# Kernel tuning notes

Hardware: AMD Instinct MI355X
Metric: run time of the kernel (lower is better)

The kernel has to match this reference:

```python
import jax, jax.numpy as jnp
import numpy as np

N_NODES = 50000
N_EDGES = 800000
IN_DIM = 128
HID = 256
NUM_GRAPHS = 128


def setup_inputs() -> dict:
    key = jax.random.key(0)
    ks = jax.random.split(key, 12)
    x = jax.random.normal(ks[0], (N_NODES, IN_DIM), dtype=jnp.float32)
    edge_index = jax.random.randint(ks[1], (2, N_EDGES), 0, N_NODES, dtype=jnp.int32)
    batch = jnp.sort(jax.random.randint(ks[2], (N_NODES,), 0, NUM_GRAPHS, dtype=jnp.int32))
    def glorot(k, fan_in, fan_out):
        s = jnp.sqrt(6.0 / (fan_in + fan_out))
        return jax.random.uniform(k, (fan_in, fan_out), jnp.float32, -s, s)
    W1 = glorot(ks[3], IN_DIM, HID); b1 = jnp.zeros((HID,), jnp.float32)
    W2 = glorot(ks[4], HID, HID);    b2 = jnp.zeros((HID,), jnp.float32)
    W3 = glorot(ks[5], HID, HID // 2); b3 = jnp.zeros((HID // 2,), jnp.float32)
    W4 = glorot(ks[6], HID // 2, 1);   b4 = jnp.zeros((1,), jnp.float32)
    return {"x": x, "edge_index": edge_index, "batch": batch,
            "W1": W1, "b1": b1, "W2": W2, "b2": b2,
            "W3": W3, "b3": b3, "W4": W4, "b4": b4}


def _gcn_conv(x, src, dst, dinv, W, b, n_nodes):
    # x: [N, F_in] -> [N, F_out]; PyG GCNConv: xW gathered at src, scaled by
    # symmetric norm deg^-1/2[src]*deg^-1/2[dst], scatter-added at dst, + bias.
    h = x @ W                                   # [N, F_out]
    norm = dinv[src] * dinv[dst]                # [E+N]
    msg = h[src] * norm[:, None]                # [E+N, F_out]
    return jax.ops.segment_sum(msg, dst, num_segments=n_nodes) + b


def reference(x, edge_index, batch, W1, b1, W2, b2, W3, b3, W4, b4):
    n = x.shape[0]
    loop = jnp.arange(n, dtype=edge_index.dtype)
    src = jnp.concatenate([edge_index[0], loop])   # add self-loops
    dst = jnp.concatenate([edge_index[1], loop])
    deg = jax.ops.segment_sum(jnp.ones(src.shape[0], x.dtype), dst, num_segments=n)
    dinv = jnp.where(deg > 0, jax.lax.rsqrt(jnp.maximum(deg, 1.0)), 0.0)

    h1 = jax.nn.relu(_gcn_conv(x, src, dst, dinv, W1, b1, n))
    h2 = jax.nn.relu(_gcn_conv(h1, src, dst, dinv, W2, b2, n))

    # global_mean_pool over graph ids
    sums = jax.ops.segment_sum(h2, batch, num_segments=NUM_GRAPHS)          # [G, H]
    cnts = jax.ops.segment_sum(jnp.ones(n, h2.dtype), batch, num_segments=NUM_GRAPHS)
    g = sums / jnp.maximum(cnts, 1.0)[:, None]

    # classifier: Linear->ReLU->(Dropout eval=identity)->Linear->Sigmoid
    z = jax.nn.relu(g @ W3 + b3)
    return jax.nn.sigmoid(z @ W4 + b4)            # [G, 1]
```

## Files before the change

kernel.cpp:

```cpp
#include <hip/hip_runtime.h>
#include <math.h>

#define HID 256
#define INDIM 128
#define NPASS 8

typedef short s16x8 __attribute__((ext_vector_type(8)));
typedef float f32x4 __attribute__((ext_vector_type(4)));
typedef float f32x2 __attribute__((ext_vector_type(2)));

static __device__ __forceinline__ unsigned short f2bf(float f) {
    unsigned int u = __float_as_uint(f);
    unsigned int r = (u + 0x7fffu + ((u >> 16) & 1u)) >> 16;
    return (unsigned short)r;
}

#define DECWP(a, base, w)                                                  \
    do {                                                                   \
        a[(base) + 0] += __builtin_amdgcn_cvt_pk_f32_fp8((int)(w), false); \
        a[(base) + 1] += __builtin_amdgcn_cvt_pk_f32_fp8((int)(w), true);  \
    } while (0)
#define DEC16P(a, u)                                                       \
    do { DECWP(a, 0, (u).x); DECWP(a, 2, (u).y);                           \
         DECWP(a, 4, (u).z); DECWP(a, 6, (u).w); } while (0)

__global__ void k_count(const int* __restrict__ dst, int E, int* cnt) {
    int e = blockIdx.x * blockDim.x + threadIdx.x;
    if (e < E) atomicAdd(&cnt[dst[e]], 1);
}

__global__ __launch_bounds__(256) void k_scan_block(const int* __restrict__ cnt,
                                                    int* excl_tmp, int* blksum, int n) {
    __shared__ int sm[256];
    int t = threadIdx.x;
    int i = blockIdx.x * 256 + t;
    int c = (i < n) ? cnt[i] : 0;
    sm[t] = c;
    __syncthreads();
    for (int off = 1; off < 256; off <<= 1) {
        int v = (t >= off) ? sm[t - off] : 0;
        __syncthreads();
        sm[t] += v;
        __syncthreads();
    }
    if (i < n) excl_tmp[i] = sm[t] - c;
    if (t == 255) blksum[blockIdx.x] = sm[255];
}

__global__ __launch_bounds__(256) void k_scan_top(int* blksum, int nb) {
    __shared__ int sm[256];
    int t = threadIdx.x;
    int c = (t < nb) ? blksum[t] : 0;
    sm[t] = c;
    __syncthreads();
    for (int off = 1; off < 256; off <<= 1) {
        int v = (t >= off) ? sm[t - off] : 0;
        __syncthreads();
        sm[t] += v;
        __syncthreads();
    }
    if (t < nb) blksum[t] = sm[t] - c;
}

__global__ __launch_bounds__(256) void k_finalize_rows(const int* __restrict__ excl_tmp,
                                                       const int* __restrict__ blksum,
                                                       const int* __restrict__ cnt,
                                                       int* row_start, int* cursor,
                                                       float* dinv, int n, int E) {
    int i = blockIdx.x * 256 + threadIdx.x;
    if (i < n) {
        int r = excl_tmp[i] + blksum[blockIdx.x];
        row_start[i] = r;
        cursor[i] = r;
        dinv[i] = rsqrtf((float)(cnt[i] + 1));
    }
    if (i == 0) row_start[n] = E;
}

__global__ void k_fill(const int* __restrict__ src, const int* __restrict__ dst,
                       int E, int* cursor, int* __restrict__ csr_src, int n) {
    int e0 = blockIdx.x * blockDim.x + threadIdx.x;
    int stride = gridDim.x * blockDim.x;
    int range = (n + NPASS - 1) / NPASS;
#pragma unroll 1
    for (int p = 0; p < NPASS; p++) {
        int lo = p * range;
        int hi = lo + range;
        for (int e = e0; e < E; e += stride) {
            int d = dst[e];
            if (d >= lo && d < hi) {
                int pos = atomicAdd(&cursor[d], 1);
                csr_src[pos] = src[e];
            }
        }
    }
}

__global__ void k_cast_q(const float* __restrict__ x, const float* __restrict__ dinv,
                         unsigned int* __restrict__ out, int nw) {
    int i = blockIdx.x * blockDim.x + threadIdx.x;
    if (i < nw) {
        float dv = dinv[i >> 5];
        float4 v = ((const float4*)x)[i];
        int w0 = __builtin_amdgcn_cvt_pk_fp8_f32(v.x * dv, v.y * dv, 0, false);
        w0 = __builtin_amdgcn_cvt_pk_fp8_f32(v.z * dv, v.w * dv, w0, true);
        out[i] = (unsigned int)w0;
    }
}

template <int K>
__global__ void k_wtf(const float* __restrict__ W, uint4* __restrict__ Wfrag) {
    constexpr int NK = K / 32;
    int c_tile = blockIdx.x / NK;
    int kk = blockIdx.x % NK;
    int lane = threadIdx.x;
    int c = c_tile * 16 + (lane & 15);
    int k0 = kk * 32 + (lane >> 4) * 8;
    unsigned short b[8];
#pragma unroll
    for (int j = 0; j < 8; j++) b[j] = f2bf(W[(size_t)(k0 + j) * HID + c]);
    uint4 o;
    o.x = (unsigned int)b[0] | ((unsigned int)b[1] << 16);
    o.y = (unsigned int)b[2] | ((unsigned int)b[3] << 16);
    o.z = (unsigned int)b[4] | ((unsigned int)b[5] << 16);
    o.w = (unsigned int)b[6] | ((unsigned int)b[7] << 16);
    Wfrag[(size_t)(c_tile * NK + kk) * 64 + lane] = o;
}

template <int K, int EPI>
__global__ __launch_bounds__(256) void k_gemm_mfma(const unsigned short* __restrict__ Xb,
                                                   const uint4* __restrict__ Wfrag,
                                                   const float* __restrict__ epi,
                                                   void* __restrict__ Yout, int n) {
    constexpr int NK = K / 32;
    __shared__ uint4 bl[4 * NK * 64];

    const int nb = blockIdx.x & 3;
    const int mb = blockIdx.x >> 2;
    const int r0 = mb * 128;
    const int w = threadIdx.x >> 6;
    const int lane = threadIdx.x & 63;
    const int ar = lane & 15;
    const int ak = (lane >> 4) * 8;

    {
        const uint4* gsrc = Wfrag + (size_t)nb * 4 * NK * 64;
        for (int i = threadIdx.x; i < 4 * NK * 64; i += 256) bl[i] = gsrc[i];
    }

    int arow[2];
#pragma unroll
    for (int rt = 0; rt < 2; rt++) {
        int r = r0 + w * 32 + rt * 16 + ar;
        arow[rt] = (r < n) ? r : n - 1;
    }

    f32x4 acc[2][4];
#pragma unroll
    for (int rt = 0; rt < 2; rt++)
#pragma unroll
        for (int ct = 0; ct < 4; ct++) acc[rt][ct] = f32x4{0, 0, 0, 0};

    __syncthreads();

    s16x8 a_cur[2], a_nxt[2];
#pragma unroll
    for (int rt = 0; rt < 2; rt++)
        a_cur[rt] = *(const s16x8*)(Xb + (size_t)arow[rt] * K + ak);

#pragma unroll
    for (int kk = 0; kk < NK; kk++) {
        if (kk + 1 < NK) {
#pragma unroll
            for (int rt = 0; rt < 2; rt++)
                a_nxt[rt] = *(const s16x8*)(Xb + (size_t)arow[rt] * K + (kk + 1) * 32 + ak);
        }
        s16x8 bfrag[4];
#pragma unroll
        for (int ct = 0; ct < 4; ct++)
            bfrag[ct] = ((const s16x8*)bl)[(ct * NK + kk) * 64 + lane];
#pragma unroll
        for (int rt = 0; rt < 2; rt++)
#pragma unroll
            for (int ct = 0; ct < 4; ct++)
                acc[rt][ct] = __builtin_amdgcn_mfma_f32_16x16x32_bf16(a_cur[rt], bfrag[ct],
                                                                      acc[rt][ct], 0, 0, 0);
#pragma unroll
        for (int rt = 0; rt < 2; rt++) a_cur[rt] = a_nxt[rt];
    }

#pragma unroll
    for (int rt = 0; rt < 2; rt++) {
        int rbase = r0 + w * 32 + rt * 16 + (lane >> 4) * 4;
        if constexpr (EPI == 1) {
            unsigned short* Yb = (unsigned short*)Yout;
#pragma unroll
            for (int ct = 0; ct < 4; ct++) {
                int c = nb * 64 + ct * 16 + ar;
                float bc = epi[c];
#pragma unroll
                for (int j = 0; j < 4; j++) {
                    int r = rbase + j;
                    if (r < n) Yb[(size_t)r * HID + c] = f2bf(fmaxf(acc[rt][ct][j] + bc, 0.0f));
                }
            }
        } else {
            unsigned char* Yq = (unsigned char*)Yout;
            float dv[4];
#pragma unroll
            for (int j = 0; j < 4; j++) dv[j] = (rbase + j < n) ? epi[rbase + j] : 0.0f;
#pragma unroll
            for (int ct = 0; ct < 4; ct++) {
                int c = nb * 64 + ct * 16 + ar;
#pragma unroll
                for (int j = 0; j < 4; j++) {
                    int r = rbase + j;
                    if (r < n) {
                        float f = acc[rt][ct][j] * dv[j];
                        int e = __builtin_amdgcn_cvt_pk_fp8_f32(f, f, 0, false);
                        Yq[(size_t)r * HID + c] = (unsigned char)(e & 0xff);
                    }
                }
            }
        }
    }
}

template <int D, bool BIASRELU>
__global__ __launch_bounds__(256) void k_agg_q(const unsigned char* __restrict__ Hq,
                                               const float* __restrict__ dinv,
                                               const int* __restrict__ row_start,
                                               const int* __restrict__ csr_src,
                                               const float* __restrict__ bias,
                                               unsigned short* __restrict__ O, int n) {
    constexpr int LPR = D / 16;
    constexpr int EPW = 64 / LPR;
    const int v = blockIdx.x * 4 + (threadIdx.x >> 6);
    const int lane = threadIdx.x & 63;
    const int sub = lane / LPR;
    const int li = lane % LPR;
    if (v >= n) return;
    const uint4* H4 = (const uint4*)Hq;
    f32x2 a[8];
#pragma unroll
    for (int k = 0; k < 8; k++) a[k] = f32x2{0.f, 0.f};
    const int beg = row_start[v], end = row_start[v + 1];
    const int last = end - 1;
    for (int i = beg + sub; i < end; i += 4 * EPW) {
        int j1 = i + EPW, j2 = i + 2 * EPW, j3 = i + 3 * EPW;
        int s0 = csr_src[i];
        int t1 = csr_src[j1 <= last ? j1 : last];
        int t2 = csr_src[j2 <= last ? j2 : last];
        int t3 = csr_src[j3 <= last ? j3 : last];
        int s1 = (j1 < end) ? t1 : n;
        int s2 = (j2 < end) ? t2 : n;
        int s3 = (j3 < end) ? t3 : n;
        uint4 u0 = H4[(size_t)s0 * LPR + li];
        uint4 u1 = H4[(size_t)s1 * LPR + li];
        uint4 u2 = H4[(size_t)s2 * LPR + li];
        uint4 u3 = H4[(size_t)s3 * LPR + li];
        DEC16P(a, u0); DEC16P(a, u1); DEC16P(a, u2); DEC16P(a, u3);
    }
#pragma unroll
    for (int off = LPR; off < 64; off <<= 1)
#pragma unroll
        for (int k = 0; k < 8; k++) {
            a[k][0] += __shfl_xor(a[k][0], off);
            a[k][1] += __shfl_xor(a[k][1], off);
        }

    if (lane < LPR) {
        uint4 us = H4[(size_t)v * LPR + li];
        DEC16P(a, us);
        float dv = dinv[v];
        float o[16];
        if constexpr (BIASRELU) {
            const float4* B4 = (const float4*)bias;
#pragma unroll
            for (int q = 0; q < 4; q++) {
                float4 bb = B4[li * 4 + q];
                o[q * 4 + 0] = fmaxf(fmaf(dv, a[q * 2 + 0][0], bb.x), 0.f);
                o[q * 4 + 1] = fmaxf(fmaf(dv, a[q * 2 + 0][1], bb.y), 0.f);
                o[q * 4 + 2] = fmaxf(fmaf(dv, a[q * 2 + 1][0], bb.z), 0.f);
                o[q * 4 + 3] = fmaxf(fmaf(dv, a[q * 2 + 1][1], bb.w), 0.f);
            }
        } else {
#pragma unroll
            for (int k = 0; k < 8; k++) {
                o[k * 2 + 0] = dv * a[k][0];
                o[k * 2 + 1] = dv * a[k][1];
            }
        }
        uint4 ow0, ow1;
        ow0.x = (unsigned int)f2bf(o[0]) | ((unsigned int)f2bf(o[1]) << 16);
        ow0.y = (unsigned int)f2bf(o[2]) | ((unsigned int)f2bf(o[3]) << 16);
        ow0.z = (unsigned int)f2bf(o[4]) | ((unsigned int)f2bf(o[5]) << 16);
        ow0.w = (unsigned int)f2bf(o[6]) | ((unsigned int)f2bf(o[7]) << 16);
        ow1.x = (unsigned int)f2bf(o[8]) | ((unsigned int)f2bf(o[9]) << 16);
        ow1.y = (unsigned int)f2bf(o[10]) | ((unsigned int)f2bf(o[11]) << 16);
        ow1.z = (unsigned int)f2bf(o[12]) | ((unsigned int)f2bf(o[13]) << 16);
        ow1.w = (unsigned int)f2bf(o[14]) | ((unsigned int)f2bf(o[15]) << 16);
        uint4* Op = (uint4*)O + (size_t)v * (2 * LPR) + li * 2;
        Op[0] = ow0;
        Op[1] = ow1;
    }
}

#define BFLO(x) __uint_as_float((x) << 16)
#define BFHI(x) __uint_as_float((x) & 0xffff0000u)
#define ACC8(a, u)                                  \
    do {                                            \
        a[0] += BFLO((u).x); a[1] += BFHI((u).x);   \
        a[2] += BFLO((u).y); a[3] += BFHI((u).y);   \
        a[4] += BFLO((u).z); a[5] += BFHI((u).z);   \
        a[6] += BFLO((u).w); a[7] += BFHI((u).w);   \
    } while (0)

__global__ __launch_bounds__(256) void k_pool(const unsigned short* __restrict__ Hb,
                                              const int* __restrict__ batch,
                                              int n, float* __restrict__ G) {
    int g = blockIdx.x;
    int w = threadIdx.x >> 6;
    int lane = threadIdx.x & 63;
    int sub = lane >> 5;
    int li = lane & 31;
    int lo = 0, hi = n;
    while (lo < hi) { int m = (lo + hi) >> 1; if (batch[m] < g) lo = m + 1; else hi = m; }
    int start = lo;
    hi = n;
    while (lo < hi) { int m = (lo + hi) >> 1; if (batch[m] <= g) lo = m + 1; else hi = m; }
    int end = lo;
    const uint4* H4 = (const uint4*)Hb;
    float a[8] = {0, 0, 0, 0, 0, 0, 0, 0};
    for (int v = start + w * 2 + sub; v < end; v += 8) {
        uint4 u = H4[(size_t)v * 32 + li];
        ACC8(a, u);
    }
#pragma unroll
    for (int k = 0; k < 8; k++) a[k] += __shfl_xor(a[k], 32);
    __shared__ float red[4][32][8];
    if (lane < 32) {
#pragma unroll
        for (int k = 0; k < 8; k++) red[w][li][k] = a[k];
    }
    __syncthreads();
    if (w == 0 && lane < 32) {
        float inv = 1.0f / fmaxf((float)(end - start), 1.0f);
        float o[8];
#pragma unroll
        for (int k = 0; k < 8; k++)
            o[k] = (red[0][li][k] + red[1][li][k] + red[2][li][k] + red[3][li][k]) * inv;
        float4* Gp = (float4*)(G + (size_t)g * HID + li * 8);
        Gp[0] = make_float4(o[0], o[1], o[2], o[3]);
        Gp[1] = make_float4(o[4], o[5], o[6], o[7]);
    }
}

__global__ __launch_bounds__(128) void k_cls(const float* __restrict__ G,
                                             const float* __restrict__ W3,
                                             const float* __restrict__ b3,
                                             const float* __restrict__ W4,
                                             const float* __restrict__ b4,
                                             float* __restrict__ out) {
    __shared__ float gr[256];
    __shared__ float red[2];
    int g = blockIdx.x, t = threadIdx.x;
    gr[t] = G[g * 256 + t];
    gr[t + 128] = G[g * 256 + t + 128];
    __syncthreads();
    float z = b3[t];
    for (int k = 0; k < 256; k++) z += gr[k] * W3[k * 128 + t];
    z = fmaxf(z, 0.0f);
    float p = z * W4[t];
    for (int off = 32; off; off >>= 1) p += __shfl_down(p, off);
    if ((t & 63) == 0) red[t >> 6] = p;
    __syncthreads();
    if (t == 0) {
        float tot = red[0] + red[1] + b4[0];
        out[g] = 1.0f / (1.0f + expf(-tot));
    }
}

extern "C" void kernel_launch(void* const* d_in, const int* in_sizes, int n_in,
                              void* d_out, int out_size, void* d_ws, size_t ws_size,
                              hipStream_t stream) {
    const float* x  = (const float*)d_in[0];
    const int*   ei = (const int*)d_in[1];
    const int*   batch = (const int*)d_in[2];
    const float* W1 = (const float*)d_in[3];
    const float* b1 = (const float*)d_in[4];
    const float* W2 = (const float*)d_in[5];
    const float* b2 = (const float*)d_in[6];
    const float* W3 = (const float*)d_in[7];
    const float* b3 = (const float*)d_in[8];
    const float* W4 = (const float*)d_in[9];
    const float* b4 = (const float*)d_in[10];

    const int N = in_sizes[2];
    const int E = in_sizes[1] / 2;
    const int G = out_size;
    const int NB = (N + 255) / 256;

    char* w = (char*)d_ws;
    float* dinv      = (float*)w;  w += ((size_t)N * 4 + 255) & ~(size_t)255;
    int*   cnt       = (int*)w;    w += ((size_t)N * 4 + 255) & ~(size_t)255;
    int*   excl_tmp  = (int*)w;    w += ((size_t)N * 4 + 255) & ~(size_t)255;
    int*   blksum    = (int*)w;    w += 256 * 4;
    int*   row_start = (int*)w;    w += ((size_t)(N + 1) * 4 + 255) & ~(size_t)255;
    int*   cursor    = (int*)w;    w += ((size_t)N * 4 + 255) & ~(size_t)255;
    int*   csr_src   = (int*)w;    w += ((size_t)E * 4 + 255) & ~(size_t)255;
    unsigned char*  xq   = (unsigned char*)w;   w += ((size_t)(N + 1) * INDIM + 255) & ~(size_t)255;
    unsigned char*  Hq   = (unsigned char*)w;   w += ((size_t)(N + 1) * HID + 255) & ~(size_t)255;
    uint4* wf1 = (uint4*)w;  w += ((size_t)INDIM * HID * 2 + 255) & ~(size_t)255;
    uint4* wf2 = (uint4*)w;  w += ((size_t)HID * HID * 2 + 255) & ~(size_t)255;
    unsigned short* bufA = (unsigned short*)w;  w += (size_t)N * INDIM * 2;
    unsigned short* bufB = (unsigned short*)w;  w += (size_t)N * HID * 2;
    float* gbuf      = (float*)w;  w += (size_t)G * HID * 4;

    const int* src = ei;
    const int* dst = ei + E;

    hipMemsetAsync(xq + (size_t)N * INDIM, 0, INDIM, stream);
    hipMemsetAsync(Hq + (size_t)N * HID, 0, HID, stream);

    k_wtf<INDIM><<<16 * (INDIM / 32), 64, 0, stream>>>(W1, wf1);
    k_wtf<HID><<<16 * (HID / 32), 64, 0, stream>>>(W2, wf2);

    hipMemsetAsync(cnt, 0, (size_t)N * 4, stream);
    k_count<<<(E + 255) / 256, 256, 0, stream>>>(dst, E, cnt);
    k_scan_block<<<NB, 256, 0, stream>>>(cnt, excl_tmp, blksum, N);
    k_scan_top<<<1, 256, 0, stream>>>(blksum, NB);
    k_finalize_rows<<<NB, 256, 0, stream>>>(excl_tmp, blksum, cnt, row_start, cursor, dinv, N, E);
    k_fill<<<(E + 255) / 256, 256, 0, stream>>>(src, dst, E, cursor, csr_src, N);

    int nw = N * INDIM / 4;
    k_cast_q<<<(nw + 255) / 256, 256, 0, stream>>>(x, dinv, (unsigned int*)xq, nw);

    const int gemm_blocks = ((N + 127) / 128) * 4;
    const int agg_blocks  = (N + 3) / 4;

    k_agg_q<INDIM, false><<<agg_blocks, 256, 0, stream>>>(xq, dinv, row_start, csr_src, nullptr, bufA, N);
    k_gemm_mfma<INDIM, 1><<<gemm_blocks, 256, 0, stream>>>(bufA, wf1, b1, bufB, N);

    k_gemm_mfma<HID, 2><<<gemm_blocks, 256, 0, stream>>>(bufB, wf2, dinv, Hq, N);
    k_agg_q<HID, true><<<agg_blocks, 256, 0, stream>>>(Hq, dinv, row_start, csr_src, b2, bufB, N);

    k_pool<<<G, 256, 0, stream>>>(bufB, batch, N, gbuf);
    k_cls<<<G, 128, 0, stream>>>(gbuf, W3, b3, W4, b4, (float*)d_out);
}
```

Baseline: 256.0 us.

## Partition count and fill atomics by destination range across XCDs

Count and fill now launch 8×128 blocks. Consecutive block IDs map to 8 destination-node ranges, presumably so each XCD (given round-robin dispatch) handles atomics on one slice of cnt/cursor and those stay local to its L2. Each block scans one 1/128 slice of the edges and keeps only the edges whose destination falls in its range. This replaces the previous 8 sequential passes in fill with one parallel launch, but every edge index is now read 8 times in total and the code depends on an assumed block-to-XCD mapping.

```diff
diff --git a/kernel.cpp b/kernel.cpp
--- a/kernel.cpp
+++ b/kernel.cpp
@@ -3,7 +3,8 @@
 
 #define HID 256
 #define INDIM 128
-#define NPASS 8
+#define NXCD 8
+#define NSLICE 128
 
 typedef short s16x8 __attribute__((ext_vector_type(8)));
 typedef float f32x4 __attribute__((ext_vector_type(4)));
@@ -24,9 +25,18 @@
     do { DECWP(a, 0, (u).x); DECWP(a, 2, (u).y);                           \
          DECWP(a, 4, (u).z); DECWP(a, 6, (u).w); } while (0)
 
-__global__ void k_count(const int* __restrict__ dst, int E, int* cnt) {
-    int e = blockIdx.x * blockDim.x + threadIdx.x;
-    if (e < E) atomicAdd(&cnt[dst[e]], 1);
+__global__ void k_count(const int* __restrict__ dst, int E, int* cnt, int n) {
+    int r = blockIdx.x & (NXCD - 1);
+    int s = blockIdx.x / NXCD;
+    int range = (n + NXCD - 1) / NXCD;
+    int lo = r * range, hi = lo + range;
+    int per = (E + NSLICE - 1) / NSLICE;
+    int e0 = s * per;
+    int e1 = e0 + per; if (e1 > E) e1 = E;
+    for (int e = e0 + threadIdx.x; e < e1; e += blockDim.x) {
+        int d = dst[e];
+        if (d >= lo && d < hi) atomicAdd(&cnt[d], 1);
+    }
 }
 
 __global__ __launch_bounds__(256) void k_scan_block(const int* __restrict__ cnt,
@@ -79,19 +89,18 @@
 
 __global__ void k_fill(const int* __restrict__ src, const int* __restrict__ dst,
                        int E, int* cursor, int* __restrict__ csr_src, int n) {
-    int e0 = blockIdx.x * blockDim.x + threadIdx.x;
-    int stride = gridDim.x * blockDim.x;
-    int range = (n + NPASS - 1) / NPASS;
-#pragma unroll 1
-    for (int p = 0; p < NPASS; p++) {
-        int lo = p * range;
-        int hi = lo + range;
-        for (int e = e0; e < E; e += stride) {
-            int d = dst[e];
-            if (d >= lo && d < hi) {
-                int pos = atomicAdd(&cursor[d], 1);
-                csr_src[pos] = src[e];
-            }
+    int r = blockIdx.x & (NXCD - 1);
+    int s = blockIdx.x / NXCD;
+    int range = (n + NXCD - 1) / NXCD;
+    int lo = r * range, hi = lo + range;
+    int per = (E + NSLICE - 1) / NSLICE;
+    int e0 = s * per;
+    int e1 = e0 + per; if (e1 > E) e1 = E;
+    for (int e = e0 + threadIdx.x; e < e1; e += blockDim.x) {
+        int d = dst[e];
+        if (d >= lo && d < hi) {
+            int pos = atomicAdd(&cursor[d], 1);
+            csr_src[pos] = src[e];
         }
     }
 }
@@ -427,11 +436,11 @@
     k_wtf<HID><<<16 * (HID / 32), 64, 0, stream>>>(W2, wf2);
 
     hipMemsetAsync(cnt, 0, (size_t)N * 4, stream);
-    k_count<<<(E + 255) / 256, 256, 0, stream>>>(dst, E, cnt);
+    k_count<<<NXCD * NSLICE, 256, 0, stream>>>(dst, E, cnt, N);
     k_scan_block<<<NB, 256, 0, stream>>>(cnt, excl_tmp, blksum, N);
     k_scan_top<<<1, 256, 0, stream>>>(blksum, NB);
     k_finalize_rows<<<NB, 256, 0, stream>>>(excl_tmp, blksum, cnt, row_start, cursor, dinv, N, E);
-    k_fill<<<(E + 255) / 256, 256, 0, stream>>>(src, dst, E, cursor, csr_src, N);
+    k_fill<<<NXCD * NSLICE, 256, 0, stream>>>(src, dst, E, cursor, csr_src, N);
 
     int nw = N * INDIM / 4;
     k_cast_q<<<(nw + 255) / 256, 256, 0, stream>>>(x, dinv, (unsigned int*)xq, nw);
```

Measured after the change: 253.2 us. No clear change (-1.1%).
